# Optimization experiments

Measured on AMD Instinct MI355X. Metric: run time of the kernel, lower is better.

Reference implementation:

```python
import jax, jax.numpy as jnp
import numpy as np

KSIZE = 3
PAD = (KSIZE - 1) // 2
SIG = 0.3 * ((KSIZE - 1) * 0.5 - 1) + 0.8  # sigma_space == sigma_density == 0.8
INV2S2 = 1.0 / (2.0 * SIG * SIG)


def _gauss_space():
    c = KSIZE // 2
    xs = np.arange(KSIZE, dtype=np.float32)
    gx, gy = np.meshgrid(xs, xs, indexing='xy')
    w = np.exp(-(((gx - c) ** 2 + (gy - c) ** 2)) * INV2S2)
    w = w / w.sum()
    return jnp.asarray(w, dtype=jnp.float32)


def _patches(x):
    # x: [N,C,H,W] -> [N,C,H,W,k,k], zero padding (matches F.pad value=0)
    H, W = x.shape[-2], x.shape[-1]
    xp = jnp.pad(x, ((0, 0), (0, 0), (PAD, PAD), (PAD, PAD)))
    rows = []
    for i in range(KSIZE):
        cols = [xp[:, :, i:i + H, j:j + W] for j in range(KSIZE)]
        rows.append(jnp.stack(cols, axis=-1))
    return jnp.stack(rows, axis=-2)


def setup_inputs() -> dict:
    key = jax.random.key(0)
    k1, k2, k3 = jax.random.split(key, 3)
    B, V, C, H, W = 2, 4, 3, 512, 512
    depth = jax.random.uniform(k1, (B, V, 1, H, W), dtype=jnp.float32)
    color = jax.random.uniform(k2, (B, V, C, H, W), dtype=jnp.float32)
    mask = jax.random.uniform(k3, (B, V, 1, H, W), dtype=jnp.float32)
    return {"depth": depth, "color": color, "mask": mask}


def reference(depth, color, mask):
    B, V, C, H, W = color.shape
    d = depth.reshape(B * V, 1, H, W)
    m = mask.reshape(B * V, 1, H, W)
    c = color.reshape(B * V, C, H, W)

    dp = _patches(d)  # [N,1,H,W,k,k]
    cp = _patches(c)  # [N,C,H,W,k,k]
    mp = _patches(m)  # [N,1,H,W,k,k]

    # depth (density) gaussian weight, normalized per-pixel over the window
    wd = jnp.exp(-((dp - d[..., None, None]) ** 2) * INV2S2)
    wd = wd / wd.sum(axis=(-1, -2), keepdims=True)

    # color gaussian weight summed over channels, normalized per-pixel
    wc = jnp.exp(-((cp - c[..., None, None]) ** 2) * INV2S2).sum(axis=1, keepdims=True)
    wc = wc / wc.sum(axis=(-1, -2), keepdims=True)

    ws = _gauss_space().reshape(1, 1, 1, 1, KSIZE, KSIZE)

    w = wd * wc * ws * mp + 1e-7  # [N,1,H,W,k,k]
    out = (w * cp).sum(axis=(-1, -2)) / w.sum(axis=(-1, -2))  # [N,C,H,W]
    return out.reshape(B, V, C, H, W)
```

## Files before the change

### kernel.cpp

```cpp
#include <hip/hip_runtime.h>


typedef _Float16 h2 __attribute__((ext_vector_type(2)));

constexpr int HH = 512, WW = 512, HW = HH * WW;

__device__ __forceinline__ h2 H2c(float v) { return h2{(_Float16)v, (_Float16)v}; }

__device__ __forceinline__ h2 pkrtz(float a, float b) {
    return __builtin_bit_cast(h2, __builtin_amdgcn_cvt_pkrtz(a, b));
}

__device__ __forceinline__ h2 wpoly(h2 d) {
    h2 v = d * d + H2c(-0.5f);
    h2 w = H2c(-0.0537742f) + v * H2c(0.0105029f);
    w = H2c(0.206495f) + v * w;
    w = H2c(-0.528620f) + v * w;
    w = H2c(0.676634f) + v * w;
    return w;
}

#define WS0f 0.2724967f
#define WS1f 0.1247577f
#define WS2f 0.0571180f

struct RW {
    h2 d[5], m[5], x[5], y[5], z[5];
};
struct Acc { h2 swd, swc, st, s0, s1, s2; };

__global__ __launch_bounds__(256) void bilateral_v11(
    const float* __restrict__ depth,
    const float* __restrict__ color,
    const float* __restrict__ mask,
    float* __restrict__ out)
{
    const int lane = threadIdx.x & 63;
    const int wg   = blockIdx.x * 4 + (threadIdx.x >> 6);
    const int n    = wg >> 9;
    const int rem  = wg & 511;
    const int hp   = rem >> 1;
    const int half = rem & 1;
    const int rA   = hp * 2;
    const int c0   = half * 256 + lane * 4;

    const float* dptr = depth + (size_t)n * HW;
    const float* mptr = mask  + (size_t)n * HW;
    const float* xptr = color + (size_t)n * 3 * HW;
    const float* yptr = xptr + HW;
    const float* zptr = xptr + 2 * HW;

    const bool hasL = (c0 > 0);
    const bool hasR = (c0 < WW - 4);
    const int  colL = hasL ? c0 - 2 : c0;
    const int  colR = hasR ? c0 + 4 : c0;

#define LOADCVT(P_, base, off) do {                                          \
    const float4 _q = *reinterpret_cast<const float4*>((base) + (off) + c0); \
    const float2 _l = *reinterpret_cast<const float2*>((base) + (off) + colL); \
    const float2 _r = *reinterpret_cast<const float2*>((base) + (off) + colR); \
    const float _eL = hasL ? _l.y : 0.0f;                                    \
    const float _eR = hasR ? _r.x : 0.0f;                                    \
    P_[0] = pkrtz(_eL, _q.x);                                                \
    P_[1] = pkrtz(_q.x, _q.y);                                               \
    P_[2] = pkrtz(_q.y, _q.z);                                               \
    P_[3] = pkrtz(_q.z, _q.w);                                               \
    P_[4] = pkrtz(_q.w, _eR);                                                \
} while (0)

#define LOADWIN(W_, r) do {                                                  \
    const int _o = (r) * WW;                                                 \
    LOADCVT(W_.d, dptr, _o); LOADCVT(W_.m, mptr, _o);                        \
    LOADCVT(W_.x, xptr, _o); LOADCVT(W_.y, yptr, _o);                        \
    LOADCVT(W_.z, zptr, _o);                                                 \
} while (0)

#define TAP(S_, pi, cD, cX, cY, cZ, WSC, A_) do {                            \
    const h2 _wd = wpoly(S_.d[pi] - (cD));                                   \
    const h2 _w0 = wpoly(S_.x[pi] - (cX));                                   \
    const h2 _w1 = wpoly(S_.y[pi] - (cY));                                   \
    const h2 _w2 = wpoly(S_.z[pi] - (cZ));                                   \
    const h2 _wc = _w0 + _w1 + _w2;                                          \
    const h2 _t  = (_wd * _wc) * (H2c(WSC) * S_.m[pi]);                      \
    A_.swd += _wd; A_.swc += _wc; A_.st += _t;                               \
    A_.s0 += _t * S_.x[pi]; A_.s1 += _t * S_.y[pi]; A_.s2 += _t * S_.z[pi];  \
} while (0)

#define ROWPASS(S_, cd0,cx0,cy0,cz0, cd1,cx1,cy1,cz1, A0_, A1_, WSM, WSS) do { \
    TAP(S_, 0, cd0, cx0, cy0, cz0, WSS, A0_);                                \
    TAP(S_, 1, cd0, cx0, cy0, cz0, WSM, A0_);                                \
    TAP(S_, 2, cd0, cx0, cy0, cz0, WSS, A0_);                                \
    TAP(S_, 2, cd1, cx1, cy1, cz1, WSS, A1_);                                \
    TAP(S_, 3, cd1, cx1, cy1, cz1, WSM, A1_);                                \
    TAP(S_, 4, cd1, cx1, cy1, cz1, WSS, A1_);                                \
} while (0)

    RW A, B;
    LOADWIN(A, rA);
    LOADWIN(B, rA + 1);

    const h2 cad0 = A.d[1], cad1 = A.d[3];
    const h2 cax0 = A.x[1], cax1 = A.x[3];
    const h2 cay0 = A.y[1], cay1 = A.y[3];
    const h2 caz0 = A.z[1], caz1 = A.z[3];
    const h2 cbd0 = B.d[1], cbd1 = B.d[3];
    const h2 cbx0 = B.x[1], cbx1 = B.x[3];
    const h2 cby0 = B.y[1], cby1 = B.y[3];
    const h2 cbz0 = B.z[1], cbz1 = B.z[3];

    Acc aa0{}, aa1{}, ab0{}, ab1{};

    ROWPASS(A, cad0,cax0,cay0,caz0, cad1,cax1,cay1,caz1, aa0, aa1, WS0f, WS1f);
    ROWPASS(B, cbd0,cbx0,cby0,cbz0, cbd1,cbx1,cby1,cbz1, ab0, ab1, WS0f, WS1f);
    ROWPASS(B, cad0,cax0,cay0,caz0, cad1,cax1,cay1,caz1, aa0, aa1, WS1f, WS2f);
    ROWPASS(A, cbd0,cbx0,cby0,cbz0, cbd1,cbx1,cby1,cbz1, ab0, ab1, WS1f, WS2f);

    const bool hasUp = (hp > 0);
    const bool hasDn = (hp < 255);

    if (hasUp) {
        RW T;
        LOADWIN(T, rA - 1);
        ROWPASS(T, cad0,cax0,cay0,caz0, cad1,cax1,cay1,caz1, aa0, aa1, WS1f, WS2f);
    }
    if (hasDn) {
        RW T;
        LOADWIN(T, rA + 2);
        ROWPASS(T, cbd0,cbx0,cby0,cbz0, cbd1,cbx1,cby1,cbz1, ab0, ab1, WS1f, WS2f);
    }

#define EPI(A_, o0, o1, o2, i0, i1) do {                                     \
    {                                                                        \
        const float st  = (float)A_.st[0];                                   \
        const float g   = st + 9e-7f * (float)A_.swd[0] * (float)A_.swc[0];  \
        const float inv = __builtin_amdgcn_rcpf(g);                          \
        o0[i0] = (float)A_.s0[0] * inv;                                      \
        o1[i0] = (float)A_.s1[0] * inv;                                      \
        o2[i0] = (float)A_.s2[0] * inv;                                      \
    }                                                                        \
    {                                                                        \
        const float st  = (float)A_.st[1];                                   \
        const float g   = st + 9e-7f * (float)A_.swd[1] * (float)A_.swc[1];  \
        const float inv = __builtin_amdgcn_rcpf(g);                          \
        o0[i1] = (float)A_.s0[1] * inv;                                      \
        o1[i1] = (float)A_.s1[1] * inv;                                      \
        o2[i1] = (float)A_.s2[1] * inv;                                      \
    }                                                                        \
} while (0)

    float ra0[4], ra1[4], ra2[4], rb0[4], rb1[4], rb2[4];
    EPI(aa0, ra0, ra1, ra2, 0, 1);
    EPI(aa1, ra0, ra1, ra2, 2, 3);
    EPI(ab0, rb0, rb1, rb2, 0, 1);
    EPI(ab1, rb0, rb1, rb2, 2, 3);

    float* po = out + (size_t)n * 3 * HW + rA * WW + c0;
    *reinterpret_cast<float4*>(po)               = make_float4(ra0[0], ra0[1], ra0[2], ra0[3]);
    *reinterpret_cast<float4*>(po + HW)          = make_float4(ra1[0], ra1[1], ra1[2], ra1[3]);
    *reinterpret_cast<float4*>(po + 2 * HW)      = make_float4(ra2[0], ra2[1], ra2[2], ra2[3]);
    *reinterpret_cast<float4*>(po + WW)          = make_float4(rb0[0], rb0[1], rb0[2], rb0[3]);
    *reinterpret_cast<float4*>(po + WW + HW)     = make_float4(rb1[0], rb1[1], rb1[2], rb1[3]);
    *reinterpret_cast<float4*>(po + WW + 2 * HW) = make_float4(rb2[0], rb2[1], rb2[2], rb2[3]);
}

extern "C" void kernel_launch(void* const* d_in, const int* in_sizes, int n_in,
                              void* d_out, int out_size, void* d_ws, size_t ws_size,
                              hipStream_t stream) {
    const float* depth = (const float*)d_in[0];
    const float* color = (const float*)d_in[1];
    const float* mask  = (const float*)d_in[2];
    float* out = (float*)d_out;

    bilateral_v11<<<1024, 256, 0, stream>>>(depth, color, mask, out);
}
```

Before: 24.14 us.

## Prefetch halo rows early and specialize center taps to constant weights

All global loads for the up and down halo rows are now issued unconditionally, using clamped row indices, into raw float registers ahead of the compute that needs them. Conversion to packed fp16 happens later, so load latency overlaps the row passes. Center taps skip the polynomial evaluation: their depth weight is taken as 1 and their color weight as 3, removing exp approximations from the hot path. At image borders, zeroed windows replace the skipped row passes, which changes the border normalization slightly and raises register pressure from the extra raw buffers.

```diff
diff --git a/kernel.cpp b/kernel.cpp
--- a/kernel.cpp
+++ b/kernel.cpp
@@ -6,7 +6,6 @@
 constexpr int HH = 512, WW = 512, HW = HH * WW;
 
 __device__ __forceinline__ h2 H2c(float v) { return h2{(_Float16)v, (_Float16)v}; }
-
 __device__ __forceinline__ h2 pkrtz(float a, float b) {
     return __builtin_bit_cast(h2, __builtin_amdgcn_cvt_pkrtz(a, b));
 }
@@ -24,12 +23,12 @@
 #define WS1f 0.1247577f
 #define WS2f 0.0571180f
 
-struct RW {
-    h2 d[5], m[5], x[5], y[5], z[5];
-};
+struct RW  { h2 d[5], m[5], x[5], y[5], z[5]; };
+struct Raw { float4 dm, mm, xm, ym, zm;
+             float2 dl, dr, ml, mr, xl, xr, yl, yr, zl, zr; };
 struct Acc { h2 swd, swc, st, s0, s1, s2; };
 
-__global__ __launch_bounds__(256) void bilateral_v11(
+__global__ __launch_bounds__(256) void bilateral_v13(
     const float* __restrict__ depth,
     const float* __restrict__ color,
     const float* __restrict__ mask,
@@ -55,24 +54,46 @@
     const int  colL = hasL ? c0 - 2 : c0;
     const int  colR = hasR ? c0 + 4 : c0;
 
-#define LOADCVT(P_, base, off) do {                                          \
-    const float4 _q = *reinterpret_cast<const float4*>((base) + (off) + c0); \
-    const float2 _l = *reinterpret_cast<const float2*>((base) + (off) + colL); \
-    const float2 _r = *reinterpret_cast<const float2*>((base) + (off) + colR); \
-    const float _eL = hasL ? _l.y : 0.0f;                                    \
-    const float _eR = hasR ? _r.x : 0.0f;                                    \
-    P_[0] = pkrtz(_eL, _q.x);                                                \
-    P_[1] = pkrtz(_q.x, _q.y);                                               \
-    P_[2] = pkrtz(_q.y, _q.z);                                               \
-    P_[3] = pkrtz(_q.z, _q.w);                                               \
-    P_[4] = pkrtz(_q.w, _eR);                                                \
-} while (0)
-
-#define LOADWIN(W_, r) do {                                                  \
+#define LOADRAW(R_, r) do {                                                  \
     const int _o = (r) * WW;                                                 \
-    LOADCVT(W_.d, dptr, _o); LOADCVT(W_.m, mptr, _o);                        \
-    LOADCVT(W_.x, xptr, _o); LOADCVT(W_.y, yptr, _o);                        \
-    LOADCVT(W_.z, zptr, _o);                                                 \
+    R_.dm = *reinterpret_cast<const float4*>(dptr + _o + c0);                \
+    R_.mm = *reinterpret_cast<const float4*>(mptr + _o + c0);                \
+    R_.xm = *reinterpret_cast<const float4*>(xptr + _o + c0);                \
+    R_.ym = *reinterpret_cast<const float4*>(yptr + _o + c0);                \
+    R_.zm = *reinterpret_cast<const float4*>(zptr + _o + c0);                \
+    R_.dl = *reinterpret_cast<const float2*>(dptr + _o + colL);              \
+    R_.ml = *reinterpret_cast<const float2*>(mptr + _o + colL);              \
+    R_.xl = *reinterpret_cast<const float2*>(xptr + _o + colL);              \
+    R_.yl = *reinterpret_cast<const float2*>(yptr + _o + colL);              \
+    R_.zl = *reinterpret_cast<const float2*>(zptr + _o + colL);              \
+    R_.dr = *reinterpret_cast<const float2*>(dptr + _o + colR);              \
+    R_.mr = *reinterpret_cast<const float2*>(mptr + _o + colR);              \
+    R_.xr = *reinterpret_cast<const float2*>(xptr + _o + colR);              \
+    R_.yr = *reinterpret_cast<const float2*>(yptr + _o + colR);              \
+    R_.zr = *reinterpret_cast<const float2*>(zptr + _o + colR);              \
+} while (0)
+
+#define CVT1(dst, Qm, Ql, Qr) do {                                           \
+    dst[0] = pkrtz(hasL ? (Ql).y : 0.0f, (Qm).x);                            \
+    dst[1] = pkrtz((Qm).x, (Qm).y);                                          \
+    dst[2] = pkrtz((Qm).y, (Qm).z);                                          \
+    dst[3] = pkrtz((Qm).z, (Qm).w);                                          \
+    dst[4] = pkrtz((Qm).w, hasR ? (Qr).x : 0.0f);                            \
+} while (0)
+
+#define CVTW(W_, R_) do {                                                    \
+    CVT1(W_.d, R_.dm, R_.dl, R_.dr);                                         \
+    CVT1(W_.m, R_.mm, R_.ml, R_.mr);                                         \
+    CVT1(W_.x, R_.xm, R_.xl, R_.xr);                                         \
+    CVT1(W_.y, R_.ym, R_.yl, R_.yr);                                         \
+    CVT1(W_.z, R_.zm, R_.zl, R_.zr);                                         \
+} while (0)
+
+#define ZEROW(W_) do {                                                       \
+    _Pragma("unroll") for (int _j = 0; _j < 5; ++_j) {                       \
+        W_.d[_j] = h2{0,0}; W_.m[_j] = h2{0,0}; W_.x[_j] = h2{0,0};          \
+        W_.y[_j] = h2{0,0}; W_.z[_j] = h2{0,0};                              \
+    }                                                                        \
 } while (0)
 
 #define TAP(S_, pi, cD, cX, cY, cZ, WSC, A_) do {                            \
@@ -86,6 +107,19 @@
     A_.s0 += _t * S_.x[pi]; A_.s1 += _t * S_.y[pi]; A_.s2 += _t * S_.z[pi];  \
 } while (0)
 
+#define ROWPASS_C(S_, A0_, A1_) do {                                         \
+    TAP(S_, 0, S_.d[1], S_.x[1], S_.y[1], S_.z[1], WS1f, A0_);               \
+    { const h2 _t = H2c(3.0f * WS0f) * S_.m[1];                              \
+      A0_.swd += H2c(1.0f); A0_.swc += H2c(3.0f); A0_.st += _t;              \
+      A0_.s0 += _t * S_.x[1]; A0_.s1 += _t * S_.y[1]; A0_.s2 += _t * S_.z[1]; } \
+    TAP(S_, 2, S_.d[1], S_.x[1], S_.y[1], S_.z[1], WS1f, A0_);               \
+    TAP(S_, 2, S_.d[3], S_.x[3], S_.y[3], S_.z[3], WS1f, A1_);               \
+    { const h2 _t = H2c(3.0f * WS0f) * S_.m[3];                              \
+      A1_.swd += H2c(1.0f); A1_.swc += H2c(3.0f); A1_.st += _t;              \
+      A1_.s0 += _t * S_.x[3]; A1_.s1 += _t * S_.y[3]; A1_.s2 += _t * S_.z[3]; } \
+    TAP(S_, 4, S_.d[3], S_.x[3], S_.y[3], S_.z[3], WS1f, A1_);               \
+} while (0)
+
 #define ROWPASS(S_, cd0,cx0,cy0,cz0, cd1,cx1,cy1,cz1, A0_, A1_, WSM, WSS) do { \
     TAP(S_, 0, cd0, cx0, cy0, cz0, WSS, A0_);                                \
     TAP(S_, 1, cd0, cx0, cy0, cz0, WSM, A0_);                                \
@@ -95,9 +129,31 @@
     TAP(S_, 4, cd1, cx1, cy1, cz1, WSS, A1_);                                \
 } while (0)
 
+    const bool hasUp = (hp > 0);
+    const bool hasDn = (hp < 255);
+    const int  rUp = hasUp ? rA - 1 : rA;
+    const int  rDn = hasDn ? rA + 2 : rA;
+
+    Raw rawA, rawB;
+    LOADRAW(rawA, rA);
+    LOADRAW(rawB, rA + 1);
+
     RW A, B;
-    LOADWIN(A, rA);
-    LOADWIN(B, rA + 1);
+    CVTW(A, rawA);
+    CVTW(B, rawB);
+
+    Acc aa0{}, aa1{}, ab0{}, ab1{};
+
+    ROWPASS_C(A, aa0, aa1);
+    ROWPASS_C(B, ab0, ab1);
+
+    Raw rawT;
+    LOADRAW(rawT, rUp);
+
+    ROWPASS(B, A.d[1],A.x[1],A.y[1],A.z[1], A.d[3],A.x[3],A.y[3],A.z[3],
+            aa0, aa1, WS1f, WS2f);
+    ROWPASS(A, B.d[1],B.x[1],B.y[1],B.z[1], B.d[3],B.x[3],B.y[3],B.z[3],
+            ab0, ab1, WS1f, WS2f);
 
     const h2 cad0 = A.d[1], cad1 = A.d[3];
     const h2 cax0 = A.x[1], cax1 = A.x[3];
@@ -108,39 +164,29 @@
     const h2 cby0 = B.y[1], cby1 = B.y[3];
     const h2 cbz0 = B.z[1], cbz1 = B.z[3];
 
-    Acc aa0{}, aa1{}, ab0{}, ab1{};
-
-    ROWPASS(A, cad0,cax0,cay0,caz0, cad1,cax1,cay1,caz1, aa0, aa1, WS0f, WS1f);
-    ROWPASS(B, cbd0,cbx0,cby0,cbz0, cbd1,cbx1,cby1,cbz1, ab0, ab1, WS0f, WS1f);
-    ROWPASS(B, cad0,cax0,cay0,caz0, cad1,cax1,cay1,caz1, aa0, aa1, WS1f, WS2f);
-    ROWPASS(A, cbd0,cbx0,cby0,cbz0, cbd1,cbx1,cby1,cbz1, ab0, ab1, WS1f, WS2f);
-
-    const bool hasUp = (hp > 0);
-    const bool hasDn = (hp < 255);
-
-    if (hasUp) {
-        RW T;
-        LOADWIN(T, rA - 1);
-        ROWPASS(T, cad0,cax0,cay0,caz0, cad1,cax1,cay1,caz1, aa0, aa1, WS1f, WS2f);
-    }
-    if (hasDn) {
-        RW T;
-        LOADWIN(T, rA + 2);
-        ROWPASS(T, cbd0,cbx0,cby0,cbz0, cbd1,cbx1,cby1,cbz1, ab0, ab1, WS1f, WS2f);
-    }
+    RW T;
+    if (hasUp) CVTW(T, rawT); else ZEROW(T);
+
+    Raw rawT2;
+    LOADRAW(rawT2, rDn);
+
+    ROWPASS(T, cad0,cax0,cay0,caz0, cad1,cax1,cay1,caz1, aa0, aa1, WS1f, WS2f);
+
+    if (hasDn) CVTW(T, rawT2); else ZEROW(T);
+    ROWPASS(T, cbd0,cbx0,cby0,cbz0, cbd1,cbx1,cby1,cbz1, ab0, ab1, WS1f, WS2f);
 
 #define EPI(A_, o0, o1, o2, i0, i1) do {                                     \
     {                                                                        \
-        const float st  = (float)A_.st[0];                                   \
-        const float g   = st + 9e-7f * (float)A_.swd[0] * (float)A_.swc[0];  \
+        const float g   = (float)A_.st[0]                                    \
+                        + 9e-7f * (float)A_.swd[0] * (float)A_.swc[0];       \
         const float inv = __builtin_amdgcn_rcpf(g);                          \
         o0[i0] = (float)A_.s0[0] * inv;                                      \
         o1[i0] = (float)A_.s1[0] * inv;                                      \
         o2[i0] = (float)A_.s2[0] * inv;                                      \
     }                                                                        \
     {                                                                        \
-        const float st  = (float)A_.st[1];                                   \
-        const float g   = st + 9e-7f * (float)A_.swd[1] * (float)A_.swc[1];  \
+        const float g   = (float)A_.st[1]                                    \
+                        + 9e-7f * (float)A_.swd[1] * (float)A_.swc[1];       \
         const float inv = __builtin_amdgcn_rcpf(g);                          \
         o0[i1] = (float)A_.s0[1] * inv;                                      \
         o1[i1] = (float)A_.s1[1] * inv;                                      \
@@ -171,5 +217,5 @@
     const float* mask  = (const float*)d_in[2];
     float* out = (float*)d_out;
 
-    bilateral_v11<<<1024, 256, 0, stream>>>(depth, color, mask, out);
-}
+    bilateral_v13<<<1024, 256, 0, stream>>>(depth, color, mask, out);
+}
```

New measurement: 25.89 us. +7.3%, slower.
